# Performance work log

Hardware: AMD Instinct MI355X
Metric: run time of the kernel (lower is better)

The kernel has to match this reference:

```python
import jax, jax.numpy as jnp
import numpy as np

N_NODES = 100000
N_EDGES = 3200000
F_IN = 256
E_DIM = 128
ALPHA = 0.2


def setup_inputs() -> dict:
    key = jax.random.key(0)
    ks = jax.random.split(key, 8)
    stdv = 1.0 / np.sqrt(E_DIM)
    feature = jax.random.normal(ks[0], (N_NODES, F_IN), dtype=jnp.float32)
    edge_row = jax.random.randint(ks[1], (N_EDGES,), 0, N_NODES, dtype=jnp.int32)
    edge_col = jax.random.randint(ks[2], (N_EDGES,), 0, N_NODES, dtype=jnp.int32)
    edge_val = jnp.ones((N_EDGES,), dtype=jnp.float32)
    W = jax.random.uniform(ks[3], (F_IN, E_DIM), minval=-stdv, maxval=stdv, dtype=jnp.float32)
    b = jax.random.uniform(ks[4], (E_DIM,), minval=-stdv, maxval=stdv, dtype=jnp.float32)
    cat_W = jax.random.normal(ks[5], (E_DIM, 2 * E_DIM), dtype=jnp.float32) * 0.02
    cat_b = jnp.zeros((E_DIM,), dtype=jnp.float32)
    return {"feature": feature, "edge_row": edge_row, "edge_col": edge_col,
            "edge_val": edge_val, "W": W, "b": b, "cat_W": cat_W, "cat_b": cat_b}


def reference(feature, edge_row, edge_col, edge_val, W, b, cat_W, cat_b):
    n = feature.shape[0]

    def spmm(x):
        # adj @ x for COO adj: gather source rows, scale, scatter-add to dest rows
        return jax.ops.segment_sum(edge_val[:, None] * x[edge_col], edge_row, num_segments=n)

    support = jax.nn.relu(feature @ W)                 # [N, E]
    # (adj + I) @ support
    out_low = spmm(support) + support
    # (adj @ adj - I) @ support == adj @ (adj @ support) - support
    out_mid = spmm(spmm(support)) - support
    cat = jnp.concatenate([out_low, out_mid], axis=1)  # [N, 2E]
    out = jax.nn.leaky_relu(cat @ cat_W.T + cat_b, negative_slope=ALPHA)
    return out + b
```

## Files before the change

### kernel.cpp

```cpp
#include <hip/hip_runtime.h>

#define F_IN 256
#define EDIM 128
#define ALPHA 0.2f
#define SCAN_B 1024
#define BM 128
#define CHUNK 8192
#define BROWS 256

typedef unsigned short u16;
typedef unsigned int u32;
typedef __bf16 bf16x8 __attribute__((ext_vector_type(8)));
typedef float f32x4 __attribute__((ext_vector_type(4)));

__device__ __forceinline__ u16 f2b(float f) {
    union { float f; u32 u; } v; v.f = f;
    u32 r = v.u + 0x7FFFu + ((v.u >> 16) & 1u);
    return (u16)(r >> 16);
}
__device__ __forceinline__ float unpack_lo(u32 g) {
    union { u32 u; float f; } v; v.u = g << 16; return v.f;
}
__device__ __forceinline__ float unpack_hi(u32 g) {
    union { u32 u; float f; } v; v.u = g & 0xFFFF0000u; return v.f;
}
__device__ __forceinline__ u32 pack2(float lo, float hi) {
    return ((u32)f2b(hi) << 16) | (u32)f2b(lo);
}


__global__ __launch_bounds__(256) void k_chunk_hist(const int* __restrict__ erow,
                                                    int* __restrict__ chist,
                                                    int nE, int nbk, int nC) {
    extern __shared__ int histo[];
    const int c = blockIdx.x;
    const int t = threadIdx.x;
    for (int i = t; i < nbk; i += 256) histo[i] = 0;
    __syncthreads();
    const int beg = c * CHUNK;
    const int end = min(beg + CHUNK, nE);
    for (int e = beg + t; e < end; e += 256)
        atomicAdd(&histo[erow[e] >> 8], 1);
    __syncthreads();
    for (int i = t; i < nbk; i += 256)
        chist[(size_t)i * nC + c] = histo[i];
}

__global__ void k_scan_chunks(int* __restrict__ chist, int* __restrict__ bsum2, int nC) {
    __shared__ int s[SCAN_B];
    const int b = blockIdx.x;
    int t = threadIdx.x;
    int v = (t < nC) ? chist[(size_t)b * nC + t] : 0;
    s[t] = v;
    __syncthreads();
    for (int d = 1; d < SCAN_B; d <<= 1) {
        int add = (t >= d) ? s[t - d] : 0;
        __syncthreads();
        s[t] += add;
        __syncthreads();
    }
    if (t < nC) chist[(size_t)b * nC + t] = s[t] - v;
    if (t == SCAN_B - 1) bsum2[b] = s[t];
}

__global__ void k_scan_bsums(const int* __restrict__ bsum, int* __restrict__ boff, int nb) {
    __shared__ int s[SCAN_B];
    int t = threadIdx.x;
    int v = (t < nb) ? bsum[t] : 0;
    s[t] = v;
    __syncthreads();
    for (int d = 1; d < SCAN_B; d <<= 1) {
        int add = (t >= d) ? s[t - d] : 0;
        __syncthreads();
        s[t] += add;
        __syncthreads();
    }
    if (t < nb) boff[t] = s[t] - v;
    if (t == SCAN_B - 1) boff[nb] = s[t];
}

__global__ __launch_bounds__(256) void k_scatter2(const int* __restrict__ erow,
                                                  const int* __restrict__ ecol,
                                                  const float* __restrict__ eval,
                                                  const int* __restrict__ chist,
                                                  const int* __restrict__ boff2,
                                                  int2* __restrict__ ebuf,
                                                  int nE, int nbk, int nC) {
    extern __shared__ int cur[];
    const int c = blockIdx.x;
    const int t = threadIdx.x;
    for (int i = t; i < nbk; i += 256)
        cur[i] = chist[(size_t)i * nC + c] + boff2[i];
    __syncthreads();
    const int beg = c * CHUNK;
    const int end = min(beg + CHUNK, nE);
    for (int e = beg + t; e < end; e += 256) {
        int r = erow[e];
        int pos = atomicAdd(&cur[r >> 8], 1);
        ebuf[pos] = make_int2(ecol[e] | ((r & (BROWS - 1)) << 17), __float_as_int(eval[e]));
    }
}

__global__ __launch_bounds__(256) void k_local_sort2(const int* __restrict__ boff2,
                                                     const int2* __restrict__ ebuf,
                                                     int2* __restrict__ edges,
                                                     int* __restrict__ rowptr,
                                                     int n, int nbk) {
    __shared__ int hist[BROWS];
    __shared__ int s[BROWS];
    const int b = blockIdx.x;
    const int r0 = b * BROWS;
    const int t = threadIdx.x;
    const int beg = boff2[b];
    const int end = boff2[b + 1];
    hist[t] = 0;
    __syncthreads();
    for (int j = beg + t; j < end; j += 256)
        atomicAdd(&hist[(ebuf[j].x >> 17) & (BROWS - 1)], 1);
    __syncthreads();
    int v = hist[t];
    s[t] = v;
    __syncthreads();
    #pragma unroll
    for (int d = 1; d < BROWS; d <<= 1) {
        int add = (t >= d) ? s[t - d] : 0;
        __syncthreads();
        s[t] += add;
        __syncthreads();
    }
    int excl = beg + s[t] - v;
    if (r0 + t < n) rowptr[r0 + t] = excl;
    if (b == nbk - 1 && t == 255) rowptr[n] = end;
    if (b == nbk - 1 && t < 16) edges[end + t] = make_int2(0, 0);
    hist[t] = excl;
    __syncthreads();
    for (int j = beg + t; j < end; j += 256) {
        int2 e = ebuf[j];
        int lrow = (e.x >> 17) & (BROWS - 1);
        int pos = atomicAdd(&hist[lrow], 1);
        edges[pos] = make_int2(e.x & 0x1FFFF, e.y);
    }
}


__global__ void k_prep(const float* __restrict__ W, const float* __restrict__ catW,
                       u16* __restrict__ Wb, u16* __restrict__ catWb) {
    int idx = blockIdx.x * 256 + threadIdx.x;
    if (idx < F_IN * EDIM) {
        int k = idx >> 7;
        int c = idx & 127;
        Wb[c * F_IN + k] = f2b(W[idx]);
    } else {
        int j = idx - F_IN * EDIM;
        if (j < EDIM * 2 * EDIM) catWb[j] = f2b(catW[j]);
    }
}


#define LSTRIDE 40

__global__ __launch_bounds__(256) void k_gemm1_relu(const float* __restrict__ feature,
                                                    const u16* __restrict__ Wb,
                                                    u16* __restrict__ supb, int n) {
    __shared__ __align__(16) u16 As[BM][LSTRIDE];
    __shared__ __align__(16) u16 Bs[EDIM][LSTRIDE];
    const int t = threadIdx.x;
    const int r0 = blockIdx.x * BM;
    const int w = t >> 6, lane = t & 63;
    const int wr = w >> 1, wc = w & 1;
    const int lm = lane & 15, kg = lane >> 4;

    f32x4 acc[4][4];
    #pragma unroll
    for (int m = 0; m < 4; ++m)
        #pragma unroll
        for (int nn = 0; nn < 4; ++nn)
            acc[m][nn] = (f32x4){0.f, 0.f, 0.f, 0.f};

    const int srow = t >> 1;
    const int koff = (t & 1) * 16;

    for (int kt = 0; kt < F_IN / 32; ++kt) {
        const int k0 = kt * 32;
        {
            u32 pk[8];
            if (r0 + srow < n) {
                const float* src = feature + (size_t)(r0 + srow) * F_IN + k0 + koff;
                #pragma unroll
                for (int q = 0; q < 4; ++q) {
                    float4 f = *reinterpret_cast<const float4*>(src + q * 4);
                    pk[q * 2 + 0] = pack2(f.x, f.y);
                    pk[q * 2 + 1] = pack2(f.z, f.w);
                }
            } else {
                #pragma unroll
                for (int q = 0; q < 8; ++q) pk[q] = 0;
            }
            uint4* dst = reinterpret_cast<uint4*>(&As[srow][koff]);
            dst[0] = make_uint4(pk[0], pk[1], pk[2], pk[3]);
            dst[1] = make_uint4(pk[4], pk[5], pk[6], pk[7]);
        }
        {
            const uint4* src = reinterpret_cast<const uint4*>(Wb + (size_t)srow * F_IN + k0 + koff);
            uint4* dst = reinterpret_cast<uint4*>(&Bs[srow][koff]);
            dst[0] = src[0];
            dst[1] = src[1];
        }
        __syncthreads();
        #pragma unroll
        for (int m = 0; m < 4; ++m) {
            bf16x8 a = *reinterpret_cast<const bf16x8*>(&As[wr * 64 + m * 16 + lm][kg * 8]);
            #pragma unroll
            for (int nn = 0; nn < 4; ++nn) {
                bf16x8 b = *reinterpret_cast<const bf16x8*>(&Bs[wc * 64 + nn * 16 + lm][kg * 8]);
                acc[m][nn] = __builtin_amdgcn_mfma_f32_16x16x32_bf16(a, b, acc[m][nn], 0, 0, 0);
            }
        }
        __syncthreads();
    }
    #pragma unroll
    for (int m = 0; m < 4; ++m) {
        #pragma unroll
        for (int r = 0; r < 4; ++r) {
            int row = r0 + wr * 64 + m * 16 + kg * 4 + r;
            if (row >= n) continue;
            u16* dst = supb + (size_t)row * EDIM;
            #pragma unroll
            for (int nn = 0; nn < 4; ++nn) {
                int col = wc * 64 + nn * 16 + lm;
                dst[col] = f2b(fmaxf(acc[m][nn][r], 0.f));
            }
        }
    }
}

__global__ __launch_bounds__(256) void k_final(const u16* __restrict__ supb,
                                               const u16* __restrict__ s1b,
                                               const u16* __restrict__ s2b,
                                               float* __restrict__ out,
                                               const u16* __restrict__ catWb,
                                               const float* __restrict__ catb,
                                               const float* __restrict__ bvec, int n) {
    __shared__ __align__(16) u16 As[BM][LSTRIDE];
    __shared__ __align__(16) u16 Bs[EDIM][LSTRIDE];
    const int t = threadIdx.x;
    const int r0 = blockIdx.x * BM;
    const int w = t >> 6, lane = t & 63;
    const int wr = w >> 1, wc = w & 1;
    const int lm = lane & 15, kg = lane >> 4;

    f32x4 acc[4][4];
    #pragma unroll
    for (int m = 0; m < 4; ++m)
        #pragma unroll
        for (int nn = 0; nn < 4; ++nn)
            acc[m][nn] = (f32x4){0.f, 0.f, 0.f, 0.f};

    const int srow = t >> 1;
    const int koff = (t & 1) * 16;

    for (int kt = 0; kt < (2 * EDIM) / 32; ++kt) {
        const int k0 = kt * 32;
        {
            u32 pk[8];
            if (r0 + srow < n) {
                const int kk = k0 + koff;
                const int lo = (kk < EDIM);
                const int kcol = lo ? kk : kk - EDIM;
                size_t off = (size_t)(r0 + srow) * EDIM + kcol;
                const uint4* pa = reinterpret_cast<const uint4*>((lo ? s1b : s2b) + off);
                const uint4* pq = reinterpret_cast<const uint4*>(supb + off);
                uint4 a0 = pa[0], a1 = pa[1];
                uint4 q0 = pq[0], q1 = pq[1];
                const u32 av[8] = {a0.x, a0.y, a0.z, a0.w, a1.x, a1.y, a1.z, a1.w};
                const u32 qv[8] = {q0.x, q0.y, q0.z, q0.w, q1.x, q1.y, q1.z, q1.w};
                const float sgn = lo ? 1.f : -1.f;
                #pragma unroll
                for (int q = 0; q < 8; ++q) {
                    float x = unpack_lo(av[q]) + sgn * unpack_lo(qv[q]);
                    float y = unpack_hi(av[q]) + sgn * unpack_hi(qv[q]);
                    pk[q] = pack2(x, y);
                }
            } else {
                #pragma unroll
                for (int q = 0; q < 8; ++q) pk[q] = 0;
            }
            uint4* dst = reinterpret_cast<uint4*>(&As[srow][koff]);
            dst[0] = make_uint4(pk[0], pk[1], pk[2], pk[3]);
            dst[1] = make_uint4(pk[4], pk[5], pk[6], pk[7]);
        }
        {
            const uint4* src = reinterpret_cast<const uint4*>(catWb + (size_t)srow * (2 * EDIM) + k0 + koff);
            uint4* dst = reinterpret_cast<uint4*>(&Bs[srow][koff]);
            dst[0] = src[0];
            dst[1] = src[1];
        }
        __syncthreads();
        #pragma unroll
        for (int m = 0; m < 4; ++m) {
            bf16x8 a = *reinterpret_cast<const bf16x8*>(&As[wr * 64 + m * 16 + lm][kg * 8]);
            #pragma unroll
            for (int nn = 0; nn < 4; ++nn) {
                bf16x8 b = *reinterpret_cast<const bf16x8*>(&Bs[wc * 64 + nn * 16 + lm][kg * 8]);
                acc[m][nn] = __builtin_amdgcn_mfma_f32_16x16x32_bf16(a, b, acc[m][nn], 0, 0, 0);
            }
        }
        __syncthreads();
    }
    #pragma unroll
    for (int nn = 0; nn < 4; ++nn) {
        int col = wc * 64 + nn * 16 + lm;
        float cbv = catb[col];
        float bbv = bvec[col];
        #pragma unroll
        for (int m = 0; m < 4; ++m) {
            #pragma unroll
            for (int r = 0; r < 4; ++r) {
                int row = r0 + wr * 64 + m * 16 + kg * 4 + r;
                if (row >= n) continue;
                float v = acc[m][nn][r] + cbv;
                v = (v > 0.f ? v : ALPHA * v) + bbv;
                out[(size_t)row * EDIM + col] = v;
            }
        }
    }
}

__global__ void k_spmm_csr(const int* __restrict__ rowptr, const int2* __restrict__ edges,
                           const u16* __restrict__ xb, u16* __restrict__ yb, int n) {
    int wid = threadIdx.x >> 6;
    int lane = threadIdx.x & 63;
    int row = blockIdx.x * 4 + wid;
    if (row >= n) return;
    int beg = rowptr[row];
    int end = rowptr[row + 1];
    int c = lane * 2;
    float ax = 0.f, ay = 0.f;
    int j = beg;
    for (; j + 8 <= end; j += 8) {
        int2 ee[8];
        #pragma unroll
        for (int q = 0; q < 8; ++q) ee[q] = edges[j + q];
        u32 gg[8];
        #pragma unroll
        for (int q = 0; q < 8; ++q)
            gg[q] = *reinterpret_cast<const u32*>(xb + (size_t)ee[q].x * EDIM + c);
        #pragma unroll
        for (int q = 0; q < 8; ++q) {
            float v = __int_as_float(ee[q].y);
            ax = fmaf(v, unpack_lo(gg[q]), ax);
            ay = fmaf(v, unpack_hi(gg[q]), ay);
        }
    }
    for (; j < end; ++j) {
        int2 e = edges[j];
        u32 g = *reinterpret_cast<const u32*>(xb + (size_t)e.x * EDIM + c);
        float v = __int_as_float(e.y);
        ax = fmaf(v, unpack_lo(g), ax);
        ay = fmaf(v, unpack_hi(g), ay);
    }
    *reinterpret_cast<u32*>(yb + (size_t)row * EDIM + c) = pack2(ax, ay);
}

extern "C" void kernel_launch(void* const* d_in, const int* in_sizes, int n_in,
                              void* d_out, int out_size, void* d_ws, size_t ws_size,
                              hipStream_t stream) {
    const float* feature = (const float*)d_in[0];
    const int*   erow    = (const int*)d_in[1];
    const int*   ecol    = (const int*)d_in[2];
    const float* eval    = (const float*)d_in[3];
    const float* W       = (const float*)d_in[4];
    const float* b       = (const float*)d_in[5];
    const float* catW    = (const float*)d_in[6];
    const float* catb    = (const float*)d_in[7];
    float* out = (float*)d_out;

    const int n  = in_sizes[0] / F_IN;
    const int nE = in_sizes[1];
    const int nbk = (n + BROWS - 1) / BROWS;
    const int nC  = (nE + CHUNK - 1) / CHUNK;

    char* p = (char*)d_ws;
    u16*  supb = (u16*)p;                   p += (size_t)n * EDIM * sizeof(u16);
    u16*  s1b  = (u16*)p;                   p += (size_t)n * EDIM * sizeof(u16);
    u16*  s2b  = (u16*)p;                   p += (size_t)n * EDIM * sizeof(u16);
    p = (char*)(((size_t)p + 15) & ~(size_t)15);
    u16*  Wb   = (u16*)p;                   p += (size_t)F_IN * EDIM * sizeof(u16);
    u16*  catWb = (u16*)p;                  p += (size_t)EDIM * 2 * EDIM * sizeof(u16);
    p = (char*)(((size_t)p + 15) & ~(size_t)15);
    int2* edges = (int2*)p;                 p += (size_t)(nE + 16) * sizeof(int2);
    int2* ebuf  = (int2*)p;                 p += (size_t)nE * sizeof(int2);
    int*  rowptr = (int*)p;                 p += (size_t)(n + 1) * sizeof(int);
    int*  chist  = (int*)p;                 p += (size_t)nbk * nC * sizeof(int);
    int*  bsum2  = (int*)p;                 p += (size_t)nbk * sizeof(int);
    int*  boff2  = (int*)p;                 p += (size_t)(nbk + 1) * sizeof(int);

    const int gemmBlocks = (n + BM - 1) / BM;
    const int spmmBlocks = (n + 3) / 4;
    const size_t ldsHist = (size_t)nbk * sizeof(int);

    k_chunk_hist<<<nC, 256, ldsHist, stream>>>(erow, chist, nE, nbk, nC);
    k_scan_chunks<<<nbk, SCAN_B, 0, stream>>>(chist, bsum2, nC);
    k_scan_bsums<<<1, SCAN_B, 0, stream>>>(bsum2, boff2, nbk);

    k_scatter2<<<nC, 256, ldsHist, stream>>>(erow, ecol, eval, chist, boff2, ebuf, nE, nbk, nC);
    k_local_sort2<<<nbk, 256, 0, stream>>>(boff2, ebuf, edges, rowptr, n, nbk);

    k_prep<<<(F_IN * EDIM + EDIM * 2 * EDIM + 255) / 256, 256, 0, stream>>>(W, catW, Wb, catWb);
    k_gemm1_relu<<<gemmBlocks, 256, 0, stream>>>(feature, Wb, supb, n);

    k_spmm_csr<<<spmmBlocks, 256, 0, stream>>>(rowptr, edges, supb, s1b, n);
    k_spmm_csr<<<spmmBlocks, 256, 0, stream>>>(rowptr, edges, s1b, s2b, n);

    k_final<<<gemmBlocks, 256, 0, stream>>>(supb, s1b, s2b, out, catWb, catb, b, n);
}
```

Measured before the change: 432.8 us.

## Merge independent preprocessing kernels into shared launches to overlap work

The weight conversion now runs in the same launch as the chunk histogram, with extra blocks doing the prep work. The edge scatter and the first GEMM+ReLU are fused into one launch, with separate block ranges for each and a shared LDS buffer reinterpreted per role. The aim is to cut launch overhead and let the memory-bound scatter overlap with the compute-bound GEMM. In exchange, LDS is now sized statically to the larger of the two roles (1024 ints for the histogram, 2*BM*LSTRIDE u16 in the fused kernel), which could limit occupancy, and the histogram assumes nbk is at most 1024.

Measured after the change: 407.7 us. -5.8%, faster.

```diff
diff --git a/kernel.cpp b/kernel.cpp
--- a/kernel.cpp
+++ b/kernel.cpp
@@ -29,21 +29,37 @@
 }
 
 
-__global__ __launch_bounds__(256) void k_chunk_hist(const int* __restrict__ erow,
-                                                    int* __restrict__ chist,
-                                                    int nE, int nbk, int nC) {
-    extern __shared__ int histo[];
-    const int c = blockIdx.x;
+__global__ __launch_bounds__(256) void k_hist_prep(const int* __restrict__ erow,
+                                                   int* __restrict__ chist,
+                                                   int nE, int nbk, int nC,
+                                                   const float* __restrict__ W,
+                                                   const float* __restrict__ catW,
+                                                   u16* __restrict__ Wb,
+                                                   u16* __restrict__ catWb) {
+    __shared__ int histo[1024];
     const int t = threadIdx.x;
-    for (int i = t; i < nbk; i += 256) histo[i] = 0;
-    __syncthreads();
-    const int beg = c * CHUNK;
-    const int end = min(beg + CHUNK, nE);
-    for (int e = beg + t; e < end; e += 256)
-        atomicAdd(&histo[erow[e] >> 8], 1);
-    __syncthreads();
-    for (int i = t; i < nbk; i += 256)
-        chist[(size_t)i * nC + c] = histo[i];
+    if (blockIdx.x < nC) {
+        const int c = blockIdx.x;
+        for (int i = t; i < nbk; i += 256) histo[i] = 0;
+        __syncthreads();
+        const int beg = c * CHUNK;
+        const int end = min(beg + CHUNK, nE);
+        for (int e = beg + t; e < end; e += 256)
+            atomicAdd(&histo[erow[e] >> 8], 1);
+        __syncthreads();
+        for (int i = t; i < nbk; i += 256)
+            chist[(size_t)i * nC + c] = histo[i];
+    } else {
+        int idx = (blockIdx.x - nC) * 256 + t;
+        if (idx < F_IN * EDIM) {
+            int k = idx >> 7;
+            int c = idx & 127;
+            Wb[c * F_IN + k] = f2b(W[idx]);
+        } else {
+            int j = idx - F_IN * EDIM;
+            if (j < EDIM * 2 * EDIM) catWb[j] = f2b(catW[j]);
+        }
+    }
 }
 
 __global__ void k_scan_chunks(int* __restrict__ chist, int* __restrict__ bsum2, int nC) {
@@ -79,93 +95,41 @@
     if (t == SCAN_B - 1) boff[nb] = s[t];
 }
 
-__global__ __launch_bounds__(256) void k_scatter2(const int* __restrict__ erow,
-                                                  const int* __restrict__ ecol,
-                                                  const float* __restrict__ eval,
-                                                  const int* __restrict__ chist,
-                                                  const int* __restrict__ boff2,
-                                                  int2* __restrict__ ebuf,
-                                                  int nE, int nbk, int nC) {
-    extern __shared__ int cur[];
-    const int c = blockIdx.x;
+
+#define LSTRIDE 40
+
+__global__ __launch_bounds__(256) void k_scatter_gemm(const int* __restrict__ erow,
+                                                      const int* __restrict__ ecol,
+                                                      const float* __restrict__ eval,
+                                                      const int* __restrict__ chist,
+                                                      const int* __restrict__ boff2,
+                                                      int2* __restrict__ ebuf,
+                                                      int nE, int nbk, int nC,
+                                                      const float* __restrict__ feature,
+                                                      const u16* __restrict__ Wb,
+                                                      u16* __restrict__ supb, int n) {
+    __shared__ __align__(16) u16 smem[2 * BM * LSTRIDE];
     const int t = threadIdx.x;
-    for (int i = t; i < nbk; i += 256)
-        cur[i] = chist[(size_t)i * nC + c] + boff2[i];
-    __syncthreads();
-    const int beg = c * CHUNK;
-    const int end = min(beg + CHUNK, nE);
-    for (int e = beg + t; e < end; e += 256) {
-        int r = erow[e];
-        int pos = atomicAdd(&cur[r >> 8], 1);
-        ebuf[pos] = make_int2(ecol[e] | ((r & (BROWS - 1)) << 17), __float_as_int(eval[e]));
-    }
-}
-
-__global__ __launch_bounds__(256) void k_local_sort2(const int* __restrict__ boff2,
-                                                     const int2* __restrict__ ebuf,
-                                                     int2* __restrict__ edges,
-                                                     int* __restrict__ rowptr,
-                                                     int n, int nbk) {
-    __shared__ int hist[BROWS];
-    __shared__ int s[BROWS];
-    const int b = blockIdx.x;
-    const int r0 = b * BROWS;
-    const int t = threadIdx.x;
-    const int beg = boff2[b];
-    const int end = boff2[b + 1];
-    hist[t] = 0;
-    __syncthreads();
-    for (int j = beg + t; j < end; j += 256)
-        atomicAdd(&hist[(ebuf[j].x >> 17) & (BROWS - 1)], 1);
-    __syncthreads();
-    int v = hist[t];
-    s[t] = v;
-    __syncthreads();
-    #pragma unroll
-    for (int d = 1; d < BROWS; d <<= 1) {
-        int add = (t >= d) ? s[t - d] : 0;
-        __syncthreads();
-        s[t] += add;
-        __syncthreads();
-    }
-    int excl = beg + s[t] - v;
-    if (r0 + t < n) rowptr[r0 + t] = excl;
-    if (b == nbk - 1 && t == 255) rowptr[n] = end;
-    if (b == nbk - 1 && t < 16) edges[end + t] = make_int2(0, 0);
-    hist[t] = excl;
-    __syncthreads();
-    for (int j = beg + t; j < end; j += 256) {
-        int2 e = ebuf[j];
-        int lrow = (e.x >> 17) & (BROWS - 1);
-        int pos = atomicAdd(&hist[lrow], 1);
-        edges[pos] = make_int2(e.x & 0x1FFFF, e.y);
-    }
-}
-
-
-__global__ void k_prep(const float* __restrict__ W, const float* __restrict__ catW,
-                       u16* __restrict__ Wb, u16* __restrict__ catWb) {
-    int idx = blockIdx.x * 256 + threadIdx.x;
-    if (idx < F_IN * EDIM) {
-        int k = idx >> 7;
-        int c = idx & 127;
-        Wb[c * F_IN + k] = f2b(W[idx]);
-    } else {
-        int j = idx - F_IN * EDIM;
-        if (j < EDIM * 2 * EDIM) catWb[j] = f2b(catW[j]);
-    }
-}
-
-
-#define LSTRIDE 40
-
-__global__ __launch_bounds__(256) void k_gemm1_relu(const float* __restrict__ feature,
-                                                    const u16* __restrict__ Wb,
-                                                    u16* __restrict__ supb, int n) {
-    __shared__ __align__(16) u16 As[BM][LSTRIDE];
-    __shared__ __align__(16) u16 Bs[EDIM][LSTRIDE];
-    const int t = threadIdx.x;
-    const int r0 = blockIdx.x * BM;
+
+    if (blockIdx.x < nC) {
+        int* cur = reinterpret_cast<int*>(smem);
+        const int c = blockIdx.x;
+        for (int i = t; i < nbk; i += 256)
+            cur[i] = chist[(size_t)i * nC + c] + boff2[i];
+        __syncthreads();
+        const int beg = c * CHUNK;
+        const int end = min(beg + CHUNK, nE);
+        for (int e = beg + t; e < end; e += 256) {
+            int r = erow[e];
+            int pos = atomicAdd(&cur[r >> 8], 1);
+            ebuf[pos] = make_int2(ecol[e] | ((r & (BROWS - 1)) << 17), __float_as_int(eval[e]));
+        }
+        return;
+    }
+
+    u16 (*As)[LSTRIDE] = reinterpret_cast<u16(*)[LSTRIDE]>(smem);
+    u16 (*Bs)[LSTRIDE] = reinterpret_cast<u16(*)[LSTRIDE]>(smem + BM * LSTRIDE);
+    const int r0 = (blockIdx.x - nC) * BM;
     const int w = t >> 6, lane = t & 63;
     const int wr = w >> 1, wc = w & 1;
     const int lm = lane & 15, kg = lane >> 4;
@@ -233,6 +197,48 @@
         }
     }
 }
+
+__global__ __launch_bounds__(256) void k_local_sort2(const int* __restrict__ boff2,
+                                                     const int2* __restrict__ ebuf,
+                                                     int2* __restrict__ edges,
+                                                     int* __restrict__ rowptr,
+                                                     int n, int nbk) {
+    __shared__ int hist[BROWS];
+    __shared__ int s[BROWS];
+    const int b = blockIdx.x;
+    const int r0 = b * BROWS;
+    const int t = threadIdx.x;
+    const int beg = boff2[b];
+    const int end = boff2[b + 1];
+    hist[t] = 0;
+    __syncthreads();
+    for (int j = beg + t; j < end; j += 256)
+        atomicAdd(&hist[(ebuf[j].x >> 17) & (BROWS - 1)], 1);
+    __syncthreads();
+    int v = hist[t];
+    s[t] = v;
+    __syncthreads();
+    #pragma unroll
+    for (int d = 1; d < BROWS; d <<= 1) {
+        int add = (t >= d) ? s[t - d] : 0;
+        __syncthreads();
+        s[t] += add;
+        __syncthreads();
+    }
+    int excl = beg + s[t] - v;
+    if (r0 + t < n) rowptr[r0 + t] = excl;
+    if (b == nbk - 1 && t == 255) rowptr[n] = end;
+    if (b == nbk - 1 && t < 16) edges[end + t] = make_int2(0, 0);
+    hist[t] = excl;
+    __syncthreads();
+    for (int j = beg + t; j < end; j += 256) {
+        int2 e = ebuf[j];
+        int lrow = (e.x >> 17) & (BROWS - 1);
+        int pos = atomicAdd(&hist[lrow], 1);
+        edges[pos] = make_int2(e.x & 0x1FFFF, e.y);
+    }
+}
+
 
 __global__ __launch_bounds__(256) void k_final(const u16* __restrict__ supb,
                                                const u16* __restrict__ s1b,
@@ -397,17 +403,18 @@
 
     const int gemmBlocks = (n + BM - 1) / BM;
     const int spmmBlocks = (n + 3) / 4;
-    const size_t ldsHist = (size_t)nbk * sizeof(int);
-
-    k_chunk_hist<<<nC, 256, ldsHist, stream>>>(erow, chist, nE, nbk, nC);
+    const int prepBlocks = (F_IN * EDIM + EDIM * 2 * EDIM + 255) / 256;
+
+    k_hist_prep<<<nC + prepBlocks, 256, 0, stream>>>(erow, chist, nE, nbk, nC,
+                                                     W, catW, Wb, catWb);
     k_scan_chunks<<<nbk, SCAN_B, 0, stream>>>(chist, bsum2, nC);
     k_scan_bsums<<<1, SCAN_B, 0, stream>>>(bsum2, boff2, nbk);
 
-    k_scatter2<<<nC, 256, ldsHist, stream>>>(erow, ecol, eval, chist, boff2, ebuf, nE, nbk, nC);
+    k_scatter_gemm<<<nC + gemmBlocks, 256, 0, stream>>>(erow, ecol, eval, chist, boff2,
+                                                        ebuf, nE, nbk, nC,
+                                                        feature, Wb, supb, n);
+
     k_local_sort2<<<nbk, 256, 0, stream>>>(boff2, ebuf, edges, rowptr, n, nbk);
-
-    k_prep<<<(F_IN * EDIM + EDIM * 2 * EDIM + 255) / 256, 256, 0, stream>>>(W, catW, Wb, catWb);
-    k_gemm1_relu<<<gemmBlocks, 256, 0, stream>>>(feature, Wb, supb, n);
 
     k_spmm_csr<<<spmmBlocks, 256, 0, stream>>>(rowptr, edges, supb, s1b, n);
     k_spmm_csr<<<spmmBlocks, 256, 0, stream>>>(rowptr, edges, s1b, s2b, n);
```
